# Performance work log

Measured on AMD Instinct MI355X. Metric: run time of the kernel, lower is better.

The kernel has to match this reference:

```python
import jax, jax.numpy as jnp
import numpy as np
import math

B = 8; SEQ = 1000; C_IN = 32; D = 512; H = 8; DK = 64; DV = 64
DFF = 2048; NL = 4; ARY = 4; INNER = 5


def get_mask_np(seq_size, ary, inner):
    # full k-ary tree sizes (padded) and effective sizes per scale
    full = 1
    while full < seq_size:
        full *= ary
    all_size = [full]; effe = [seq_size]
    while all_size[-1] > 1:
        all_size.append(all_size[-1] // ary)
        effe.append(math.ceil(effe[-1] / ary))
    n = sum(all_size)
    allow = np.zeros((n, n), dtype=bool)
    w = inner // 2
    starts = np.concatenate([[0], np.cumsum(all_size)]).astype(int)
    # intra-scale local window
    for l, sz in enumerate(all_size):
        s = starts[l]
        for i in range(sz):
            lo = max(i - w, 0); hi = min(i + w + 1, sz)
            allow[s + i, s + lo:s + hi] = True
    # inter-scale parent<->children links
    for l in range(1, len(all_size)):
        s = starts[l]; ps = starts[l - 1]
        for i in range(all_size[l]):
            lo = ps + i * ary; hi = ps + (i + 1) * ary
            allow[s + i, lo:hi] = True
            allow[lo:hi, s + i] = True
    return allow, all_size, effe

ALLOW_NP, ALL_SIZE, EFFE_SIZE = get_mask_np(SEQ, ARY, INNER)
NTOT = sum(ALL_SIZE)   # 1365
DEPTH = len(ALL_SIZE)  # 6
OFFS = np.concatenate([[0], np.cumsum(ALL_SIZE)]).astype(int)


def sinusoid_pe(length, d):
    pos = np.arange(length)[:, None].astype(np.float64)
    i = np.arange(d)[None, :]
    ang = pos / np.power(10000.0, (2 * (i // 2)) / d)
    pe = np.zeros((length, d), np.float32)
    pe[:, 0::2] = np.sin(ang[:, 0::2]); pe[:, 1::2] = np.cos(ang[:, 1::2])
    return pe

PE_NP = sinusoid_pe(SEQ, D)


def layer_norm(x, s, b, eps=1e-5):
    m = x.mean(-1, keepdims=True)
    v = ((x - m) ** 2).mean(-1, keepdims=True)
    return (x - m) * jax.lax.rsqrt(v + eps) * s + b


def setup_inputs() -> dict:
    key = jax.random.key(0)
    ks = jax.random.split(key, 10)
    p = lambda k, shape, sc=0.02: jax.random.normal(k, shape, jnp.float32) * sc
    return {
        "x": jax.random.normal(ks[0], (B, SEQ, C_IN), jnp.float32),
        "conv_w": p(ks[1], (D, C_IN, 3), 0.05),
        "norm_s": jnp.ones((D,), jnp.float32), "norm_b": jnp.zeros((D,), jnp.float32),
        "wq": p(ks[2], (NL, D, H * DK)), "wk": p(ks[3], (NL, D, H * DK)),
        "wv": p(ks[4], (NL, D, H * DV)), "wo": p(ks[5], (NL, H * DV, D)),
        "ln1_s": jnp.ones((NL, D), jnp.float32), "ln1_b": jnp.zeros((NL, D), jnp.float32),
        "w1": p(ks[6], (NL, D, DFF)), "b1": jnp.zeros((NL, DFF), jnp.float32),
        "w2": p(ks[7], (NL, DFF, D)), "b2": jnp.zeros((NL, D), jnp.float32),
        "ln2_s": jnp.ones((NL, D), jnp.float32), "ln2_b": jnp.zeros((NL, D), jnp.float32),
    }


def reference(x, conv_w, norm_s, norm_b, wq, wk, wv, wo, ln1_s, ln1_b,
              w1, b1, w2, b2, ln2_s, ln2_b):
    allow = jnp.asarray(ALLOW_NP)        # [N,N] True = attend
    pe = jnp.asarray(PE_NP)              # [S,D]
    # --- DataEmbedding: conv1d(k=3, circular pad, no bias) + sinusoid PE ---
    xt = jnp.concatenate([x[:, -1:], x, x[:, :1]], axis=1)       # (B,S+2,C)
    emb = jax.lax.conv_general_dilated(
        xt, conv_w, (1,), 'VALID', dimension_numbers=('NWC', 'OIW', 'NWC'))
    emb = emb + pe[None]                                          # (B,S,D)
    # pad sequence to full-tree leaf count
    emb = jnp.pad(emb, ((0, 0), (0, ALL_SIZE[0] - SEQ), (0, 0)))  # (B,L0,D)
    # --- MaxPooling_Construct: pool by ary per level, concat, LayerNorm ---
    parts = [emb]
    cur = emb
    for lvl in range(DEPTH - 1):
        L = cur.shape[1]
        cur = cur.reshape(B, L // ARY, ARY, D).max(axis=2)
        parts.append(cur)
    seq = jnp.concatenate(parts, axis=1)                          # (B,N,D)
    seq = layer_norm(seq, norm_s, norm_b)
    # --- masked MHA encoder layers (post-norm) ---
    scale = 1.0 / math.sqrt(DK)
    neg = jnp.float32(-1e9)
    for l in range(NL):
        q = (seq @ wq[l]).reshape(B, NTOT, H, DK)
        k = (seq @ wk[l]).reshape(B, NTOT, H, DK)
        v = (seq @ wv[l]).reshape(B, NTOT, H, DV)
        scores = jnp.einsum('bnhd,bmhd->bhnm', q, k) * scale
        scores = jnp.where(allow[None, None], scores, neg)
        attn = jax.nn.softmax(scores, axis=-1)
        ctx = jnp.einsum('bhnm,bmhd->bnhd', attn, v).reshape(B, NTOT, H * DV)
        seq = layer_norm(seq + ctx @ wo[l], ln1_s[l], ln1_b[l])
        ff = jax.nn.gelu(seq @ w1[l] + b1[l], approximate=False) @ w2[l] + b2[l]
        seq = layer_norm(seq + ff, ln2_s[l], ln2_b[l])
    # --- keep only the effective (unpadded) prefix of each scale ---
    out = jnp.concatenate(
        [seq[:, OFFS[i]:OFFS[i] + EFFE_SIZE[i]] for i in range(DEPTH)], axis=1)
    return out  # (B, sum(effe)=1334, D)
```

## Files before the change

### kernel.cpp

```cpp
#include <hip/hip_runtime.h>
#include <cstdint>
#include <math.h>

#define DEV __device__ __forceinline__

static constexpr int BQ = 8, SEQN = 1000, CIN = 32, NH = 8;
static constexpr int NLAY = 4;
static constexpr int NTOT_C = 1365;
static constexpr int M_REAL = BQ * NTOT_C;
static constexpr int M_PAD  = 11008;

DEV float bf2f(unsigned short u){ return __uint_as_float(((unsigned)u) << 16); }
DEV unsigned short f2bf(float f){
  unsigned u = __float_as_uint(f);
  u += 0x7fffu + ((u >> 16) & 1u);
  return (unsigned short)(u >> 16);
}

typedef __bf16 bf16x8 __attribute__((ext_vector_type(8)));
typedef float  f32x4  __attribute__((ext_vector_type(4)));
typedef unsigned short u16x8 __attribute__((ext_vector_type(8)));

#define GLD_LDS16(gp, lp) __builtin_amdgcn_global_load_lds( \
    (const __attribute__((address_space(1))) void*)(gp), \
    (__attribute__((address_space(3))) void*)(lp), 16, 0, 0)

template<int N> DEV void waitcnt_vm(){
  asm volatile("s_waitcnt vmcnt(%0)" :: "i"(N) : "memory");
}
DEV void waitcnt_lgkm0(){ asm volatile("s_waitcnt lgkmcnt(0)" ::: "memory"); }
DEV void cfence(){ asm volatile("" ::: "memory"); }

DEV float gelu_f(float x){
  float z = 0.7978845608028654f * (x + 0.044715f * x * x * x);
  z = fminf(fmaxf(z, -10.f), 10.f);
  float e = __expf(2.f * z);
  float th = (e - 1.f) / (e + 1.f);
  return 0.5f * x * (1.f + th);
}

__global__ __launch_bounds__(256) void pe_kernel(float* __restrict__ pe)
{
  int idx = blockIdx.x * 256 + threadIdx.x;
  int d = idx & 511, s = idx >> 9;
  if (s >= SEQN) return;
  float e2 = (float)(d & ~1);
  float freq = exp2f(e2 * (-13.287712379549449f / 512.0f));
  float ang = (float)s * freq;
  pe[idx] = (d & 1) ? cosf(ang) : sinf(ang);
}

__global__ __launch_bounds__(256) void conv_kernel(const float* __restrict__ x,
    const float* __restrict__ w, const float* __restrict__ pe, float* __restrict__ seqf)
{
  __shared__ float ws_w[128 * 97];
  __shared__ __align__(16) float xs[66][32];
  int b = blockIdx.z, s0 = blockIdx.y * 64, d0 = blockIdx.x * 128;
  int tid = threadIdx.x;
  for (int i = tid; i < 128 * 96; i += 256){
    int r = i / 96, c = i - r * 96;
    ws_w[r * 97 + c] = w[(size_t)(d0 + r) * 96 + c];
  }
  for (int i = tid; i < 66 * 32; i += 256){
    int r = i >> 5, c = i & 31;
    int ss = s0 + r - 1;
    ss = (ss < 0) ? (ss + SEQN) : (ss >= SEQN ? ss - SEQN : ss);
    xs[r][c] = x[((size_t)b * SEQN + ss) * CIN + c];
  }
  __syncthreads();
  int dl = tid & 127, sh = tid >> 7;
  float wr[96];
  #pragma unroll
  for (int i = 0; i < 96; i++) wr[i] = ws_w[dl * 97 + i];
  int d = d0 + dl;
  for (int si = 0; si < 32; si++){
    int sl = sh * 32 + si;
    int s = s0 + sl;
    float acc = 0.f;
    #pragma unroll
    for (int kk = 0; kk < 3; kk++){
      const float* xr = xs[sl + kk];
      #pragma unroll
      for (int c = 0; c < 32; c++) acc += xr[c] * wr[c * 3 + kk];
    }
    float outv = (s < SEQN) ? acc + pe[(size_t)s * 512 + d] : 0.f;
    seqf[((size_t)b * NTOT_C + s) * 512 + d] = outv;
  }
}

__global__ __launch_bounds__(256) void pool_kernel(float* __restrict__ seqf,
    int inOff, int outOff, int outSz)
{
  int e = blockIdx.x * 256 + threadIdx.x;
  int d = e & 511;
  int r = e >> 9;
  int i = r % outSz;
  int b = r / outSz;
  const float* src = seqf + ((size_t)b * NTOT_C + inOff + 4 * i) * 512 + d;
  float m = fmaxf(fmaxf(src[0], src[512]), fmaxf(src[1024], src[1536]));
  seqf[((size_t)b * NTOT_C + outOff + i) * 512 + d] = m;
}

__global__ __launch_bounds__(256) void ln4_kernel(const float* __restrict__ xin,
    unsigned short* __restrict__ outb,
    const float* __restrict__ sg, const float* __restrict__ bg, int M)
{
  int row = blockIdx.x * 4 + (threadIdx.x >> 6);
  int lane = threadIdx.x & 63;
  size_t base = (size_t)row * 512 + lane * 8;
  if (row >= M){
    u16x8 z8 = {0, 0, 0, 0, 0, 0, 0, 0};
    *reinterpret_cast<u16x8*>(outb + base) = z8;
    return;
  }
  f32x4 v0 = *reinterpret_cast<const f32x4*>(xin + base);
  f32x4 v1 = *reinterpret_cast<const f32x4*>(xin + base + 4);
  float sall = v0[0] + v0[1] + v0[2] + v0[3] + v1[0] + v1[1] + v1[2] + v1[3];
  #pragma unroll
  for (int o = 32; o; o >>= 1) sall += __shfl_xor(sall, o, 64);
  float mean = sall * (1.f / 512.f);
  float d[8];
  #pragma unroll
  for (int e = 0; e < 4; e++){ d[e] = v0[e] - mean; d[4 + e] = v1[e] - mean; }
  float sq = 0.f;
  #pragma unroll
  for (int e = 0; e < 8; e++) sq += d[e] * d[e];
  #pragma unroll
  for (int o = 32; o; o >>= 1) sq += __shfl_xor(sq, o, 64);
  float rstd = 1.f / sqrtf(sq * (1.f / 512.f) + 1e-5f);
  f32x4 s0 = *reinterpret_cast<const f32x4*>(sg + lane * 8);
  f32x4 s1 = *reinterpret_cast<const f32x4*>(sg + lane * 8 + 4);
  f32x4 g0 = *reinterpret_cast<const f32x4*>(bg + lane * 8);
  f32x4 g1 = *reinterpret_cast<const f32x4*>(bg + lane * 8 + 4);
  u16x8 yb;
  #pragma unroll
  for (int e = 0; e < 4; e++){
    yb[e]     = f2bf(d[e] * rstd * s0[e] + g0[e]);
    yb[4 + e] = f2bf(d[4 + e] * rstd * s1[e] + g1[e]);
  }
  *reinterpret_cast<u16x8*>(outb + base) = yb;
}

template<int MODE>
__global__ __launch_bounds__(256) void lnres4_kernel(const unsigned short* __restrict__ cin,
    unsigned short* __restrict__ seqb, float* __restrict__ out,
    const float* __restrict__ sg, const float* __restrict__ bg, int M)
{
  int row = blockIdx.x * 4 + (threadIdx.x >> 6);
  int lane = threadIdx.x & 63;
  size_t base = (size_t)row * 512 + lane * 8;
  if (row >= M){
    if (MODE == 0){
      u16x8 z8 = {0, 0, 0, 0, 0, 0, 0, 0};
      *reinterpret_cast<u16x8*>(seqb + base) = z8;
    }
    return;
  }
  u16x8 cv = *reinterpret_cast<const u16x8*>(cin + base);
  u16x8 rv = *reinterpret_cast<const u16x8*>(seqb + base);
  float v[8];
  #pragma unroll
  for (int e = 0; e < 8; e++) v[e] = bf2f(cv[e]) + bf2f(rv[e]);
  float sall = 0.f;
  #pragma unroll
  for (int e = 0; e < 8; e++) sall += v[e];
  #pragma unroll
  for (int o = 32; o; o >>= 1) sall += __shfl_xor(sall, o, 64);
  float mean = sall * (1.f / 512.f);
  float sq = 0.f;
  #pragma unroll
  for (int e = 0; e < 8; e++){ v[e] -= mean; sq += v[e] * v[e]; }
  #pragma unroll
  for (int o = 32; o; o >>= 1) sq += __shfl_xor(sq, o, 64);
  float rstd = 1.f / sqrtf(sq * (1.f / 512.f) + 1e-5f);
  f32x4 s0 = *reinterpret_cast<const f32x4*>(sg + lane * 8);
  f32x4 s1 = *reinterpret_cast<const f32x4*>(sg + lane * 8 + 4);
  f32x4 g0 = *reinterpret_cast<const f32x4*>(bg + lane * 8);
  f32x4 g1 = *reinterpret_cast<const f32x4*>(bg + lane * 8 + 4);
  f32x4 y0, y1;
  #pragma unroll
  for (int e = 0; e < 4; e++){
    y0[e] = v[e] * rstd * s0[e] + g0[e];
    y1[e] = v[4 + e] * rstd * s1[e] + g1[e];
  }
  if (MODE == 0){
    u16x8 yb;
    #pragma unroll
    for (int e = 0; e < 4; e++){ yb[e] = f2bf(y0[e]); yb[4 + e] = f2bf(y1[e]); }
    *reinterpret_cast<u16x8*>(seqb + base) = yb;
  } else {
    int b = row / NTOT_C, n = row - b * NTOT_C;
    int o;
    if      (n < 1000) o = n;
    else if (n < 1024) o = -1;
    else if (n < 1274) o = n - 24;
    else if (n < 1280) o = -1;
    else if (n < 1343) o = n - 30;
    else if (n == 1343) o = -1;
    else               o = n - 31;
    if (o >= 0){
      size_t ob = ((size_t)b * 1334 + o) * 512 + lane * 8;
      *reinterpret_cast<f32x4*>(out + ob) = y0;
      *reinterpret_cast<f32x4*>(out + ob + 4) = y1;
    }
  }
}

__global__ __launch_bounds__(256) void wconv_all(
    const float* __restrict__ wq, const float* __restrict__ wk,
    const float* __restrict__ wv, const float* __restrict__ wo,
    const float* __restrict__ w1, const float* __restrict__ w2,
    unsigned short* __restrict__ qkvT, unsigned short* __restrict__ woT,
    unsigned short* __restrict__ w1T, unsigned short* __restrict__ w2T)
{
  __shared__ float tile[32][33];
  int bid = blockIdx.x;
  const float* wl; unsigned short* wtl; int N, K, n0, k0;
  if (bid < 4096){
    int part = bid >> 10, t = bid & 1023;
    int l = t >> 8, t2 = t & 255;
    k0 = (t2 >> 4) * 32; n0 = (t2 & 15) * 32;
    N = 512; K = 512;
    const float* s = (part == 0) ? wq : (part == 1) ? wk : (part == 2) ? wv : wo;
    wl = s + (size_t)l * 512 * 512;
    wtl = (part < 3) ? (qkvT + (size_t)l * 1536 * 512 + (size_t)part * 512 * 512)
                     : (woT + (size_t)l * 512 * 512);
  } else if (bid < 8192){
    int t = bid - 4096, l = t >> 10, t2 = t & 1023;
    k0 = (t2 >> 6) * 32; n0 = (t2 & 63) * 32;
    N = 2048; K = 512;
    wl = w1 + (size_t)l * 512 * 2048;
    wtl = w1T + (size_t)l * 2048 * 512;
  } else {
    int t = bid - 8192, l = t >> 10, t2 = t & 1023;
    k0 = (t2 >> 4) * 32; n0 = (t2 & 15) * 32;
    N = 512; K = 2048;
    wl = w2 + (size_t)l * 2048 * 512;
    wtl = w2T + (size_t)l * 512 * 2048;
  }
  int c = threadIdx.x & 31, r8 = threadIdx.x >> 5;
  #pragma unroll
  for (int p = 0; p < 4; p++){ int r = r8 + p * 8; tile[r][c] = wl[(size_t)(k0 + r) * N + n0 + c]; }
  __syncthreads();
  #pragma unroll
  for (int p = 0; p < 4; p++){ int r = r8 + p * 8; wtl[(size_t)(n0 + r) * K + k0 + c] = f2bf(tile[c][r]); }
}

template<int EPI, int BM, int BN>
__global__ __launch_bounds__(256) void gemm2_kernel(
    const unsigned short* __restrict__ A, const unsigned short* __restrict__ Wt,
    unsigned short* __restrict__ Cb, const float* __restrict__ bias,
    int N, int K, int GX, int GY)
{
  constexpr int MF = BM / 32, NF = BN / 32;
  constexpr int LA = BM / 32, LB = BN / 32;
  __shared__ __align__(16) unsigned short Abuf[2][BM * 64];
  __shared__ __align__(16) unsigned short Bbuf[2][BN * 64];
  const int tid = threadIdx.x;
  const int wid = tid >> 6, lane = tid & 63;
  const int wm2 = wid >> 1, wn2 = wid & 1;
  const int r16 = lane & 15, g = lane >> 4;

  int wg = blockIdx.x;
  int group = wg / (8 * GX);
  int rem   = wg - group * 8 * GX;
  int gbase = group * 8;
  int m_t, n_t;
  if (gbase + 8 <= GY){ m_t = gbase + (rem & 7); n_t = rem >> 3; }
  else { int r = GY - gbase; m_t = gbase + rem % r; n_t = rem / r; }
  const int m0 = m_t * BM, n0 = n_t * BN;

  const int row0 = tid >> 3;
  const int scol = ((tid & 7) ^ (row0 & 7)) * 8;
  const unsigned short* gAs = A  + (size_t)(m0 + row0) * K + scol;
  const unsigned short* gBs = Wt + (size_t)(n0 + row0) * K + scol;

  const int swz0 = ((0 + g) ^ (r16 & 7)) * 8;
  const int swz1 = ((4 + g) ^ (r16 & 7)) * 8;
  const int arow = (wm2 * (BM / 2) + r16) * 64;
  const int brow = (wn2 * (BN / 2) + r16) * 64;

  const int nt = K >> 6;
  f32x4 acc[MF][NF] = {};

  auto STAGE_A = [&](int buf, int kt){
    #pragma unroll
    for (int q = 0; q < LA; q++)
      GLD_LDS16(gAs + kt * 64 + (size_t)q * 32 * K, &Abuf[buf][q * 2048 + tid * 8]);
  };
  auto STAGE_B = [&](int buf, int kt){
    #pragma unroll
    for (int q = 0; q < LB; q++)
      GLD_LDS16(gBs + kt * 64 + (size_t)q * 32 * K, &Bbuf[buf][q * 2048 + tid * 8]);
  };

  cfence();
  STAGE_A(0, 0); STAGE_B(0, 0);
  if (nt > 1){ STAGE_A(1, 1); waitcnt_vm<LA>(); }
  else        { waitcnt_vm<0>(); }
  __builtin_amdgcn_s_barrier();
  cfence();

  for (int t = 0; t < nt; t++){
    const int d = t & 1;
    const unsigned short* Ab = Abuf[d];
    const unsigned short* Bb = Bbuf[d];

    bf16x8 a0[MF], b0[NF];
    #pragma unroll
    for (int m = 0; m < MF; m++) a0[m] = *reinterpret_cast<const bf16x8*>(&Ab[arow + m * 1024 + swz0]);
    #pragma unroll
    for (int n = 0; n < NF; n++) b0[n] = *reinterpret_cast<const bf16x8*>(&Bb[brow + n * 1024 + swz0]);
    if (t + 1 < nt){ cfence(); STAGE_B(d ^ 1, t + 1); cfence(); }
    __builtin_amdgcn_s_setprio(1);
    #pragma unroll
    for (int m = 0; m < MF; m++)
      #pragma unroll
      for (int n = 0; n < NF; n++)
        acc[m][n] = __builtin_amdgcn_mfma_f32_16x16x32_bf16(a0[m], b0[n], acc[m][n], 0, 0, 0);
    __builtin_amdgcn_s_setprio(0);

    bf16x8 a1[MF], b1v[NF];
    #pragma unroll
    for (int m = 0; m < MF; m++) a1[m] = *reinterpret_cast<const bf16x8*>(&Ab[arow + m * 1024 + swz1]);
    #pragma unroll
    for (int n = 0; n < NF; n++) b1v[n] = *reinterpret_cast<const bf16x8*>(&Bb[brow + n * 1024 + swz1]);
    waitcnt_lgkm0();
    __builtin_amdgcn_s_barrier();
    cfence();
    if (t + 2 < nt){ STAGE_A(d, t + 2); cfence(); }
    __builtin_amdgcn_s_setprio(1);
    #pragma unroll
    for (int m = 0; m < MF; m++)
      #pragma unroll
      for (int n = 0; n < NF; n++)
        acc[m][n] = __builtin_amdgcn_mfma_f32_16x16x32_bf16(a1[m], b1v[n], acc[m][n], 0, 0, 0);
    __builtin_amdgcn_s_setprio(0);

    if (t + 1 < nt){
      if (t + 2 < nt) waitcnt_vm<LA>();
      else            waitcnt_vm<0>();
      __builtin_amdgcn_s_barrier();
      cfence();
    }
  }

  const int colBase = n0 + wn2 * (BN / 2) + r16;
  #pragma unroll
  for (int m = 0; m < MF; m++){
    int row = m0 + wm2 * (BM / 2) + m * 16 + g * 4;
    #pragma unroll
    for (int n = 0; n < NF; n++){
      int col = colBase + n * 16;
      float bsv = (EPI >= 2) ? bias[col] : 0.f;
      #pragma unroll
      for (int j = 0; j < 4; j++){
        float v = acc[m][n][j];
        if (EPI >= 2) v += bsv;
        if (EPI == 2) v = gelu_f(v);
        Cb[(size_t)(row + j) * N + col] = f2bf(v);
      }
    }
  }
}

__global__ __launch_bounds__(256) void attn_kernel(
    const unsigned short* __restrict__ qkv, unsigned short* __restrict__ ctx)
{
  int wid = blockIdx.x * 4 + (threadIdx.x >> 6);
  int lane = threadIdx.x & 63;
  int n = wid % NTOT_C;
  int b = wid / NTOT_C;

  int i, sz, of, cb, par;
  if (n < 1024){ i = n;        sz = 1024; of = 0;    cb = -1;            par = 1024 + (i >> 2); }
  else if (n < 1280){ i = n - 1024; sz = 256; of = 1024; cb = 0    + 4 * i; par = 1280 + (i >> 2); }
  else if (n < 1344){ i = n - 1280; sz = 64;  of = 1280; cb = 1024 + 4 * i; par = 1344 + (i >> 2); }
  else if (n < 1360){ i = n - 1344; sz = 16;  of = 1344; cb = 1280 + 4 * i; par = 1360 + (i >> 2); }
  else if (n < 1364){ i = n - 1360; sz = 4;   of = 1360; cb = 1344 + 4 * i; par = 1364; }
  else { i = 0; sz = 1; of = 1364; cb = 1360; par = -1; }

  int nb[10];
  #pragma unroll
  for (int s5 = 0; s5 < 5; s5++){ int pos = i - 2 + s5; nb[s5] = (pos >= 0 && pos < sz) ? of + pos : -1; }
  #pragma unroll
  for (int r = 0; r < 4; r++) nb[5 + r] = (cb >= 0) ? cb + r : -1;
  nb[9] = par;

  const unsigned short* rows = qkv + ((size_t)b * NTOT_C) * 1536;

  u16x8 qv = *reinterpret_cast<const u16x8*>(rows + (size_t)n * 1536 + lane * 8);
  float qf[8];
  #pragma unroll
  for (int e = 0; e < 8; e++) qf[e] = bf2f(qv[e]);

  float sc[10];
  #pragma unroll
  for (int j = 0; j < 10; j++){
    int id = nb[j] >= 0 ? nb[j] : n;
    u16x8 kv = *reinterpret_cast<const u16x8*>(rows + (size_t)id * 1536 + 512 + lane * 8);
    float p = 0.f;
    #pragma unroll
    for (int e = 0; e < 8; e++) p += qf[e] * bf2f(kv[e]);
    p += __shfl_xor(p, 1, 64);
    p += __shfl_xor(p, 2, 64);
    p += __shfl_xor(p, 4, 64);
    sc[j] = (nb[j] >= 0) ? p * 0.125f : -1e30f;
  }
  float mx = sc[0];
  #pragma unroll
  for (int j = 1; j < 10; j++) mx = fmaxf(mx, sc[j]);
  float den = 0.f;
  float wj[10];
  #pragma unroll
  for (int j = 0; j < 10; j++){
    wj[j] = (nb[j] >= 0) ? expf(sc[j] - mx) : 0.f;
    den += wj[j];
  }
  float rden = 1.f / den;
  float accv[8] = {};
  #pragma unroll
  for (int j = 0; j < 10; j++){
    int id = nb[j] >= 0 ? nb[j] : n;
    u16x8 vv = *reinterpret_cast<const u16x8*>(rows + (size_t)id * 1536 + 1024 + lane * 8);
    float w = wj[j];
    #pragma unroll
    for (int e = 0; e < 8; e++) accv[e] += w * bf2f(vv[e]);
  }
  u16x8 ov;
  #pragma unroll
  for (int e = 0; e < 8; e++) ov[e] = f2bf(accv[e] * rden);
  *reinterpret_cast<u16x8*>(ctx + ((size_t)b * NTOT_C + n) * 512 + lane * 8) = ov;
}

extern "C" void kernel_launch(void* const* d_in, const int* in_sizes, int n_in,
                              void* d_out, int out_size, void* d_ws, size_t ws_size,
                              hipStream_t stream)
{
  const float* x      = (const float*)d_in[0];
  const float* conv_w = (const float*)d_in[1];
  const float* norm_s = (const float*)d_in[2];
  const float* norm_b = (const float*)d_in[3];
  const float* wq     = (const float*)d_in[4];
  const float* wk     = (const float*)d_in[5];
  const float* wv     = (const float*)d_in[6];
  const float* wo     = (const float*)d_in[7];
  const float* ln1_s  = (const float*)d_in[8];
  const float* ln1_b  = (const float*)d_in[9];
  const float* w1     = (const float*)d_in[10];
  const float* b1     = (const float*)d_in[11];
  const float* w2     = (const float*)d_in[12];
  const float* b2     = (const float*)d_in[13];
  const float* ln2_s  = (const float*)d_in[14];
  const float* ln2_b  = (const float*)d_in[15];
  float* out = (float*)d_out;

  char* ws = (char*)d_ws;
  size_t off = 0;
  auto alloc = [&](size_t bytes) -> char* {
    char* p = ws + off; off += (bytes + 255) & ~(size_t)255; return p;
  };
  unsigned short* qkvT = (unsigned short*)alloc((size_t)NLAY * 1536 * 512 * 2);
  unsigned short* woT  = (unsigned short*)alloc((size_t)NLAY * 512 * 512 * 2);
  unsigned short* w1T  = (unsigned short*)alloc((size_t)NLAY * 2048 * 512 * 2);
  unsigned short* w2T  = (unsigned short*)alloc((size_t)NLAY * 512 * 2048 * 2);
  float*          seqf = (float*)alloc((size_t)M_PAD * 512 * 4);
  unsigned short* seqb = (unsigned short*)alloc((size_t)M_PAD * 512 * 2);
  float*          buff = (float*)alloc((size_t)M_PAD * 512 * 4);
  unsigned short* qkvb = (unsigned short*)alloc((size_t)M_PAD * 1536 * 2);
  unsigned short* ctxb = (unsigned short*)alloc((size_t)M_PAD * 512 * 2);
  unsigned short* ffn1 = qkvb;
  float*          pe   = buff;
  unsigned short* delta = (unsigned short*)buff;

  wconv_all<<<12288, 256, 0, stream>>>(wq, wk, wv, wo, w1, w2, qkvT, woT, w1T, w2T);

  pe_kernel<<<(SEQN * 512) / 256, 256, 0, stream>>>(pe);
  conv_kernel<<<dim3(4,16,BQ), 256, 0, stream>>>(x, conv_w, pe, seqf);
  const int psz[6]  = {1024, 256, 64, 16, 4, 1};
  const int poff[6] = {0, 1024, 1280, 1344, 1360, 1364};
  for (int l = 0; l < 5; l++)
    pool_kernel<<<(BQ * psz[l+1] * 512) / 256, 256, 0, stream>>>(seqf, poff[l], poff[l+1], psz[l+1]);
  ln4_kernel<<<M_PAD / 4, 256, 0, stream>>>(seqf, seqb, norm_s, norm_b, M_REAL);

  for (int l = 0; l < NLAY; l++){
    gemm2_kernel<1,128,128><<<12*86,256,0,stream>>>(seqb, qkvT + (size_t)l*1536*512, qkvb, nullptr, 1536, 512, 12, 86);
    attn_kernel<<<(BQ * NTOT_C + 3) / 4, 256, 0, stream>>>(qkvb, ctxb);
    gemm2_kernel<1,64,128><<<4*172,256,0,stream>>>(ctxb, woT + (size_t)l*512*512, delta, nullptr, 512, 512, 4, 172);
    lnres4_kernel<0><<<M_PAD / 4,256,0,stream>>>(delta, seqb, nullptr, ln1_s + l*512, ln1_b + l*512, M_REAL);
    gemm2_kernel<2,128,128><<<16*86,256,0,stream>>>(seqb, w1T + (size_t)l*2048*512, ffn1, b1 + l*2048, 2048, 512, 16, 86);
    gemm2_kernel<4,64,128><<<4*172,256,0,stream>>>(ffn1, w2T + (size_t)l*512*2048, delta, b2 + l*512, 512, 2048, 4, 172);
    if (l < NLAY - 1)
      lnres4_kernel<0><<<M_PAD / 4,256,0,stream>>>(delta, seqb, nullptr, ln2_s + l*512, ln2_b + l*512, M_REAL);
    else
      lnres4_kernel<1><<<M_PAD / 4,256,0,stream>>>(delta, seqb, out, ln2_s + l*512, ln2_b + l*512, M_REAL);
  }
}
```

Baseline: 677.0 us.

## Fuse sparse tree attention into the output projection GEMM

Replaces the separate attention kernel and Wo GEMM with one kernel. Each block computes the masked-attention context for 32 rows into swizzled LDS, then runs an MFMA GEMM against streamed, double-buffered Wo tiles. This removes the global context buffer round-trip and one launch per layer. In exchange, attention is recomputed once per output column tile, and the small M tile reduces GEMM reuse.

```diff
diff --git a/kernel.cpp b/kernel.cpp
--- a/kernel.cpp
+++ b/kernel.cpp
@@ -364,73 +364,160 @@
   }
 }
 
-__global__ __launch_bounds__(256) void attn_kernel(
-    const unsigned short* __restrict__ qkv, unsigned short* __restrict__ ctx)
-{
-  int wid = blockIdx.x * 4 + (threadIdx.x >> 6);
-  int lane = threadIdx.x & 63;
-  int n = wid % NTOT_C;
-  int b = wid / NTOT_C;
-
-  int i, sz, of, cb, par;
-  if (n < 1024){ i = n;        sz = 1024; of = 0;    cb = -1;            par = 1024 + (i >> 2); }
-  else if (n < 1280){ i = n - 1024; sz = 256; of = 1024; cb = 0    + 4 * i; par = 1280 + (i >> 2); }
-  else if (n < 1344){ i = n - 1280; sz = 64;  of = 1280; cb = 1024 + 4 * i; par = 1344 + (i >> 2); }
-  else if (n < 1360){ i = n - 1344; sz = 16;  of = 1344; cb = 1280 + 4 * i; par = 1360 + (i >> 2); }
-  else if (n < 1364){ i = n - 1360; sz = 4;   of = 1360; cb = 1344 + 4 * i; par = 1364; }
-  else { i = 0; sz = 1; of = 1364; cb = 1360; par = -1; }
-
-  int nb[10];
-  #pragma unroll
-  for (int s5 = 0; s5 < 5; s5++){ int pos = i - 2 + s5; nb[s5] = (pos >= 0 && pos < sz) ? of + pos : -1; }
-  #pragma unroll
-  for (int r = 0; r < 4; r++) nb[5 + r] = (cb >= 0) ? cb + r : -1;
-  nb[9] = par;
-
-  const unsigned short* rows = qkv + ((size_t)b * NTOT_C) * 1536;
-
-  u16x8 qv = *reinterpret_cast<const u16x8*>(rows + (size_t)n * 1536 + lane * 8);
-  float qf[8];
-  #pragma unroll
-  for (int e = 0; e < 8; e++) qf[e] = bf2f(qv[e]);
-
-  float sc[10];
-  #pragma unroll
-  for (int j = 0; j < 10; j++){
-    int id = nb[j] >= 0 ? nb[j] : n;
-    u16x8 kv = *reinterpret_cast<const u16x8*>(rows + (size_t)id * 1536 + 512 + lane * 8);
-    float p = 0.f;
-    #pragma unroll
-    for (int e = 0; e < 8; e++) p += qf[e] * bf2f(kv[e]);
-    p += __shfl_xor(p, 1, 64);
-    p += __shfl_xor(p, 2, 64);
-    p += __shfl_xor(p, 4, 64);
-    sc[j] = (nb[j] >= 0) ? p * 0.125f : -1e30f;
-  }
-  float mx = sc[0];
-  #pragma unroll
-  for (int j = 1; j < 10; j++) mx = fmaxf(mx, sc[j]);
-  float den = 0.f;
-  float wj[10];
-  #pragma unroll
-  for (int j = 0; j < 10; j++){
-    wj[j] = (nb[j] >= 0) ? expf(sc[j] - mx) : 0.f;
-    den += wj[j];
-  }
-  float rden = 1.f / den;
-  float accv[8] = {};
-  #pragma unroll
-  for (int j = 0; j < 10; j++){
-    int id = nb[j] >= 0 ? nb[j] : n;
-    u16x8 vv = *reinterpret_cast<const u16x8*>(rows + (size_t)id * 1536 + 1024 + lane * 8);
-    float w = wj[j];
-    #pragma unroll
-    for (int e = 0; e < 8; e++) accv[e] += w * bf2f(vv[e]);
-  }
-  u16x8 ov;
-  #pragma unroll
-  for (int e = 0; e < 8; e++) ov[e] = f2bf(accv[e] * rden);
-  *reinterpret_cast<u16x8*>(ctx + ((size_t)b * NTOT_C + n) * 512 + lane * 8) = ov;
+__global__ __launch_bounds__(256) void attnwo_kernel(
+    const unsigned short* __restrict__ qkv, const unsigned short* __restrict__ Wt,
+    unsigned short* __restrict__ Cb, int GX, int GY)
+{
+  __shared__ __align__(16) unsigned short ctxL[32 * 512];
+  __shared__ __align__(16) unsigned short Bbuf[2][128 * 64];
+  const int tid = threadIdx.x;
+  const int wid = tid >> 6, lane = tid & 63;
+  const int wm2 = wid >> 1, wn2 = wid & 1;
+  const int r16 = lane & 15, g = lane >> 4;
+
+  int wg = blockIdx.x;
+  int group = wg / (8 * GX);
+  int rem   = wg - group * 8 * GX;
+  int gbase = group * 8;
+  int m_t, n_t;
+  if (gbase + 8 <= GY){ m_t = gbase + (rem & 7); n_t = rem >> 3; }
+  else { int r = GY - gbase; m_t = gbase + rem % r; n_t = rem / r; }
+  const int m0 = m_t * 32, n0 = n_t * 128;
+
+  const int row0 = tid >> 3;
+  const int scol = ((tid & 7) ^ (row0 & 7)) * 8;
+  const unsigned short* gBs = Wt + (size_t)(n0 + row0) * 512 + scol;
+  cfence();
+  #pragma unroll
+  for (int q = 0; q < 4; q++) GLD_LDS16(gBs +      (size_t)q * 32 * 512, &Bbuf[0][q * 2048 + tid * 8]);
+  #pragma unroll
+  for (int q = 0; q < 4; q++) GLD_LDS16(gBs + 64 + (size_t)q * 32 * 512, &Bbuf[1][q * 2048 + tid * 8]);
+  cfence();
+
+  for (int i = 0; i < 8; i++){
+    int l = wid * 8 + i;
+    int grow = m0 + l;
+    u16x8 ov = {0, 0, 0, 0, 0, 0, 0, 0};
+    if (grow < M_REAL){
+      int b = grow / NTOT_C, n = grow - b * NTOT_C;
+      int ii, sz, of, cb, par;
+      if (n < 1024){ ii = n;        sz = 1024; of = 0;    cb = -1;             par = 1024 + (ii >> 2); }
+      else if (n < 1280){ ii = n - 1024; sz = 256; of = 1024; cb = 0    + 4 * ii; par = 1280 + (ii >> 2); }
+      else if (n < 1344){ ii = n - 1280; sz = 64;  of = 1280; cb = 1024 + 4 * ii; par = 1344 + (ii >> 2); }
+      else if (n < 1360){ ii = n - 1344; sz = 16;  of = 1344; cb = 1280 + 4 * ii; par = 1360 + (ii >> 2); }
+      else if (n < 1364){ ii = n - 1360; sz = 4;   of = 1360; cb = 1344 + 4 * ii; par = 1364; }
+      else { ii = 0; sz = 1; of = 1364; cb = 1360; par = -1; }
+
+      int nb[10];
+      #pragma unroll
+      for (int s5 = 0; s5 < 5; s5++){ int pos = ii - 2 + s5; nb[s5] = (pos >= 0 && pos < sz) ? of + pos : -1; }
+      #pragma unroll
+      for (int r = 0; r < 4; r++) nb[5 + r] = (cb >= 0) ? cb + r : -1;
+      nb[9] = par;
+
+      const unsigned short* rows = qkv + ((size_t)b * NTOT_C) * 1536;
+      u16x8 qv = *reinterpret_cast<const u16x8*>(rows + (size_t)n * 1536 + lane * 8);
+      float qf[8];
+      #pragma unroll
+      for (int e = 0; e < 8; e++) qf[e] = bf2f(qv[e]);
+
+      float sc[10];
+      #pragma unroll
+      for (int j = 0; j < 10; j++){
+        int id = nb[j] >= 0 ? nb[j] : n;
+        u16x8 kv = *reinterpret_cast<const u16x8*>(rows + (size_t)id * 1536 + 512 + lane * 8);
+        float p = 0.f;
+        #pragma unroll
+        for (int e = 0; e < 8; e++) p += qf[e] * bf2f(kv[e]);
+        p += __shfl_xor(p, 1, 64);
+        p += __shfl_xor(p, 2, 64);
+        p += __shfl_xor(p, 4, 64);
+        sc[j] = (nb[j] >= 0) ? p * 0.125f : -1e30f;
+      }
+      float mx = sc[0];
+      #pragma unroll
+      for (int j = 1; j < 10; j++) mx = fmaxf(mx, sc[j]);
+      float den = 0.f, wj[10];
+      #pragma unroll
+      for (int j = 0; j < 10; j++){
+        wj[j] = (nb[j] >= 0) ? expf(sc[j] - mx) : 0.f;
+        den += wj[j];
+      }
+      float rden = 1.f / den;
+      float accv[8] = {};
+      #pragma unroll
+      for (int j = 0; j < 10; j++){
+        int id = nb[j] >= 0 ? nb[j] : n;
+        u16x8 vv = *reinterpret_cast<const u16x8*>(rows + (size_t)id * 1536 + 1024 + lane * 8);
+        float w = wj[j];
+        #pragma unroll
+        for (int e = 0; e < 8; e++) accv[e] += w * bf2f(vv[e]);
+      }
+      #pragma unroll
+      for (int e = 0; e < 8; e++) ov[e] = f2bf(accv[e] * rden);
+    }
+    *reinterpret_cast<u16x8*>(&ctxL[l * 512 + ((lane ^ (l & 7)) * 8)]) = ov;
+  }
+  __syncthreads();
+  cfence();
+
+  const int arowL = wm2 * 16 + r16;
+  const int ax = arowL & 7;
+  const int brow = (wn2 * 64 + r16) * 64;
+  const int swz0 = ((0 + g) ^ (r16 & 7)) * 8;
+  const int swz1 = ((4 + g) ^ (r16 & 7)) * 8;
+  f32x4 acc[4] = {};
+
+  for (int t = 0; t < 8; t++){
+    const int d = t & 1;
+    const unsigned short* Bb = Bbuf[d];
+    int c0 = t * 8 + g, c1 = t * 8 + 4 + g;
+    bf16x8 a0 = *reinterpret_cast<const bf16x8*>(&ctxL[arowL * 512 + ((c0 ^ ax) * 8)]);
+    bf16x8 b0[4];
+    #pragma unroll
+    for (int n = 0; n < 4; n++) b0[n] = *reinterpret_cast<const bf16x8*>(&Bb[brow + n * 1024 + swz0]);
+    __builtin_amdgcn_s_setprio(1);
+    #pragma unroll
+    for (int n = 0; n < 4; n++)
+      acc[n] = __builtin_amdgcn_mfma_f32_16x16x32_bf16(a0, b0[n], acc[n], 0, 0, 0);
+    __builtin_amdgcn_s_setprio(0);
+
+    bf16x8 a1 = *reinterpret_cast<const bf16x8*>(&ctxL[arowL * 512 + ((c1 ^ ax) * 8)]);
+    bf16x8 b1v[4];
+    #pragma unroll
+    for (int n = 0; n < 4; n++) b1v[n] = *reinterpret_cast<const bf16x8*>(&Bb[brow + n * 1024 + swz1]);
+    waitcnt_lgkm0();
+    __builtin_amdgcn_s_barrier();
+    cfence();
+    if (t + 2 < 8){
+      #pragma unroll
+      for (int q = 0; q < 4; q++)
+        GLD_LDS16(gBs + (t + 2) * 64 + (size_t)q * 32 * 512, &Bbuf[d][q * 2048 + tid * 8]);
+      cfence();
+    }
+    __builtin_amdgcn_s_setprio(1);
+    #pragma unroll
+    for (int n = 0; n < 4; n++)
+      acc[n] = __builtin_amdgcn_mfma_f32_16x16x32_bf16(a1, b1v[n], acc[n], 0, 0, 0);
+    __builtin_amdgcn_s_setprio(0);
+
+    if (t + 1 < 8){
+      if (t + 2 < 8) waitcnt_vm<4>();
+      else           waitcnt_vm<0>();
+      __builtin_amdgcn_s_barrier();
+      cfence();
+    }
+  }
+
+  const int colBase = n0 + wn2 * 64 + r16;
+  int row = m0 + wm2 * 16 + g * 4;
+  #pragma unroll
+  for (int n = 0; n < 4; n++){
+    int col = colBase + n * 16;
+    #pragma unroll
+    for (int j = 0; j < 4; j++)
+      Cb[(size_t)(row + j) * 512 + col] = f2bf(acc[n][j]);
+  }
 }
 
 extern "C" void kernel_launch(void* const* d_in, const int* in_sizes, int n_in,
@@ -468,7 +555,6 @@
   unsigned short* seqb = (unsigned short*)alloc((size_t)M_PAD * 512 * 2);
   float*          buff = (float*)alloc((size_t)M_PAD * 512 * 4);
   unsigned short* qkvb = (unsigned short*)alloc((size_t)M_PAD * 1536 * 2);
-  unsigned short* ctxb = (unsigned short*)alloc((size_t)M_PAD * 512 * 2);
   unsigned short* ffn1 = qkvb;
   float*          pe   = buff;
   unsigned short* delta = (unsigned short*)buff;
@@ -485,8 +571,7 @@
 
   for (int l = 0; l < NLAY; l++){
     gemm2_kernel<1,128,128><<<12*86,256,0,stream>>>(seqb, qkvT + (size_t)l*1536*512, qkvb, nullptr, 1536, 512, 12, 86);
-    attn_kernel<<<(BQ * NTOT_C + 3) / 4, 256, 0, stream>>>(qkvb, ctxb);
-    gemm2_kernel<1,64,128><<<4*172,256,0,stream>>>(ctxb, woT + (size_t)l*512*512, delta, nullptr, 512, 512, 4, 172);
+    attnwo_kernel<<<4*344,256,0,stream>>>(qkvb, woT + (size_t)l*512*512, delta, 4, 344);
     lnres4_kernel<0><<<M_PAD / 4,256,0,stream>>>(delta, seqb, nullptr, ln1_s + l*512, ln1_b + l*512, M_REAL);
     gemm2_kernel<2,128,128><<<16*86,256,0,stream>>>(seqb, w1T + (size_t)l*2048*512, ffn1, b1 + l*2048, 2048, 512, 16, 86);
     gemm2_kernel<4,64,128><<<4*172,256,0,stream>>>(ffn1, w2T + (size_t)l*512*2048, delta, b2 + l*512, 512, 2048, 4, 172);
```

Result: slower. 874.6 us (+29.2%).
